# Kernel tuning notes

Hardware: AMD Instinct MI355X
Metric: run time of the kernel (lower is better)

Reference implementation:

```python
import jax, jax.numpy as jnp
import numpy as np

B = 8192
HIDDEN_DIM = 512
CODEBOOK_SIZE = 4096
ID_LENGTH = 4


def setup_inputs() -> dict:
    key = jax.random.key(0)
    kx, kc = jax.random.split(key)
    x = jax.random.normal(kx, (B, HIDDEN_DIM), dtype=jnp.float32)
    # codebooks: id_length tables of [codebook_size, hidden_dim], init ~ N(0,1) per nn.Parameter(torch.randn(...))
    codebooks = jax.random.normal(kc, (ID_LENGTH, CODEBOOK_SIZE, HIDDEN_DIM), dtype=jnp.float32)
    temperature = jnp.float32(0.05)
    return {"x": x, "temperature": temperature, "codebooks": codebooks}


def reference(x, temperature, codebooks):
    """Eval-mode forward of SemanticIDQuantizer (standard RVQ with soft/hard straight-through).
    Returns (quantized [B,D], residual_loss scalar, residuals_stack [B,L,D], codebook_usage [L,K]).
    """
    L, K, D = codebooks.shape
    temp = jnp.clip(temperature, 0.04)  # torch.clamp(temperature, min=0.04)
    residual = x
    quantized = jnp.zeros_like(x)
    residual_loss = jnp.asarray(0.0, x.dtype)
    residuals_list = []
    usage_list = []
    for i in range(L):  # small fixed layer count
        cb = codebooks[i]                                  # [K, D]
        similarity = (residual @ cb.T) / temp              # [B, K]
        hard_indices = jnp.argmax(similarity, axis=-1)     # [B]
        soft = jax.nn.softmax(similarity, axis=-1)         # [B, K]
        q_soft = soft @ cb                                 # [B, D]
        q_hard = cb[hard_indices]                          # [B, D] embedding lookup
        # straight-through: value == hard, gradient flows through soft path (and hard gather)
        q_layer = q_hard + (q_soft - jax.lax.stop_gradient(q_soft))
        residual_loss = residual_loss + jnp.mean((q_layer - residual) ** 2)
        residual = residual - q_layer
        quantized = quantized + q_layer
        residuals_list.append(residual)
        usage_list.append(jnp.zeros((K,), x.dtype).at[hard_indices].set(1.0))
    # codebook L2 regularizer: sum_i mean_k ||cb_ik||^2 * lambda / L == lambda * mean over (L,K) of ||.||^2
    codebook_reg = jnp.mean(jnp.sum(codebooks.astype(x.dtype) ** 2, axis=-1))
    residual_loss = (residual_loss + 0.01 * codebook_reg) / D
    residuals_stack = jax.lax.stop_gradient(jnp.stack(residuals_list, axis=1))  # [B, L, D]
    codebook_usage = jnp.stack(usage_list)  # [L, K]
    return quantized, residual_loss, residuals_stack, codebook_usage
```

## Files before the change

### kernel.cpp

```cpp
#include <hip/hip_runtime.h>
#include <math.h>

#define NB 8192
#define DD 512
#define KC 4096
#define NL 4

#define NTB 32
#define MARGIN_I 2048.0f
#define QS 16.0f

#define GBM 256
#define GBN 256

typedef int    i32x4 __attribute__((ext_vector_type(4)));
typedef unsigned short u16;
typedef unsigned int   u32;
typedef unsigned long long u64;

struct Top2 { float v1; int i1; float v2; int i2; };

__device__ __forceinline__ u32 umaxu(u32 a, u32 b) { return a > b ? a : b; }
__device__ __forceinline__ u32 uminu(u32 a, u32 b) { return a < b ? a : b; }

__device__ __forceinline__ u32 q8(float f) {
    int v = (int)rintf(f * QS);
    v = v < -127 ? -127 : (v > 127 ? 127 : v);
    return (u32)(v & 0xFF);
}

__global__ __launch_bounds__(256)
void k_cvt_all(const float* __restrict__ x, const float* __restrict__ cb,
               u64* __restrict__ residq, u64* __restrict__ cbq,
               double* __restrict__ cq, float* __restrict__ usage)
{
    const int bid = blockIdx.x;
    if (bid < 4096) {
        __shared__ double red[256];
        const int i = bid * 256 + threadIdx.x;
        if (bid < 64) {
            const float4 z = {0.f, 0.f, 0.f, 0.f};
            ((float4*)usage)[i] = z;
        }
        const float4 a = ((const float4*)cb)[i * 2];
        const float4 b = ((const float4*)cb)[i * 2 + 1];
        u64 p = (u64)(q8(a.x) | (q8(a.y) << 8) | (q8(a.z) << 16) | (q8(a.w) << 24))
              | ((u64)(q8(b.x) | (q8(b.y) << 8) | (q8(b.z) << 16) | (q8(b.w) << 24)) << 32);
        cbq[i] = p;
        red[threadIdx.x] = (double)a.x * a.x + (double)a.y * a.y + (double)a.z * a.z
                         + (double)a.w * a.w + (double)b.x * b.x + (double)b.y * b.y
                         + (double)b.z * b.z + (double)b.w * b.w;
        __syncthreads();
        for (int st = 128; st > 0; st >>= 1) {
            if (threadIdx.x < st) red[threadIdx.x] += red[threadIdx.x + st];
            __syncthreads();
        }
        if (threadIdx.x == 0) cq[bid] = red[0];
    } else {
        const int i = (bid - 4096) * 256 + threadIdx.x;
        const float4 a = ((const float4*)x)[i * 2];
        const float4 b = ((const float4*)x)[i * 2 + 1];
        u64 p = (u64)(q8(a.x) | (q8(a.y) << 8) | (q8(a.z) << 16) | (q8(a.w) << 24))
              | ((u64)(q8(b.x) | (q8(b.y) << 8) | (q8(b.z) << 16) | (q8(b.w) << 24)) << 32);
        residq[i] = p;
    }
}

__global__ __launch_bounds__(512, 2)
void k_simtop2(const char* __restrict__ Ri, const char* __restrict__ Ci,
               Top2* __restrict__ part )
{
    __shared__ __align__(16) char As[2][16384];
    __shared__ __align__(16) char Bs[2][16384];

    const int tid  = threadIdx.x;
    const int lane = tid & 63;
    const int w    = tid >> 6;
    const int wm   = w >> 2;
    const int wn   = w & 3;

    const int bid = blockIdx.x;
    const int xcd = bid & 7;
    const int idx = bid >> 3;
    const int row_pan  = (xcd >> 1) * 8 + (idx >> 3);
    const int col_tile = (xcd & 1) * 8 + (idx & 7);
    const int rb0 = row_pan * GBM;
    const int cb0 = col_tile * GBN;

    const int rowA = tid >> 1;
    const int h    = tid & 1;
    const int fr   = (rowA & 3) ^ ((rowA >> 2) & 3);
    const char* gAb = Ri + (size_t)(rb0 + rowA) * 512 + h * 32;
    const char* gBb = Ci + (size_t)(cb0 + rowA) * 512 + h * 32;
    const int wpos0 = rowA * 64 + (((2 * h)     ^ fr) << 4);
    const int wpos1 = rowA * 64 + (((2 * h + 1) ^ fr) << 4);

    const int la = lane & 15, ks = lane >> 4;
    const int fla = (la & 3) ^ ((la >> 2) & 3);
    const int offA = (wm * 128 + la) * 64 + ((ks ^ fla) << 4);
    const int offB = (wn * 64  + la) * 64 + ((ks ^ fla) << 4);

    i32x4 acc[8][4];
    const i32x4 zero = {0, 0, 0, 0};
#pragma unroll
    for (int m = 0; m < 8; ++m)
#pragma unroll
        for (int n = 0; n < 4; ++n) acc[m][n] = zero;

    uint4 eA0, eA1, eB0, eB1;
    uint4 oA0, oA1, oB0, oB1;

#define LOADT(rA0, rA1, rB0, rB1, T) do {                    \
        const char* _pa = gAb + (T) * 64;                    \
        rA0 = *(const uint4*)(_pa);                          \
        rA1 = *(const uint4*)(_pa + 16);                     \
        const char* _pb = gBb + (T) * 64;                    \
        rB0 = *(const uint4*)(_pb);                          \
        rB1 = *(const uint4*)(_pb + 16);                     \
    } while (0)

#define ITER(T, rA0, rA1, rB0, rB1, P) do {                               \
        *(uint4*)(&As[P][0] + wpos0) = rA0;                               \
        *(uint4*)(&As[P][0] + wpos1) = rA1;                               \
        *(uint4*)(&Bs[P][0] + wpos0) = rB0;                               \
        *(uint4*)(&Bs[P][0] + wpos1) = rB1;                               \
        if ((T) + 2 < 8) LOADT(rA0, rA1, rB0, rB1, (T) + 2);              \
        asm volatile("s_waitcnt lgkmcnt(0)" ::: "memory");                \
        __builtin_amdgcn_s_barrier();                                     \
        const char* _rA = &As[P][0];                                      \
        const char* _rB = &Bs[P][0];                                      \
        i32x4 av[8], bv[4];                                               \
        _Pragma("unroll")                                                 \
        for (int m = 0; m < 8; ++m) av[m] = *(const i32x4*)(_rA + offA + m * 1024); \
        _Pragma("unroll")                                                 \
        for (int n = 0; n < 4; ++n) bv[n] = *(const i32x4*)(_rB + offB + n * 1024); \
        _Pragma("unroll")                                                 \
        for (int m = 0; m < 8; ++m)                                       \
            _Pragma("unroll")                                             \
            for (int n = 0; n < 4; ++n)                                   \
                acc[m][n] = __builtin_amdgcn_mfma_i32_16x16x64_i8(av[m], bv[n], acc[m][n], 0, 0, 0); \
    } while (0)

    LOADT(eA0, eA1, eB0, eB1, 0);
    LOADT(oA0, oA1, oB0, oB1, 1);

#pragma unroll 1
    for (int tt = 0; tt < 8; tt += 2) {
        ITER(tt,     eA0, eA1, eB0, eB1, 0);
        ITER(tt + 1, oA0, oA1, oB0, oB1, 1);
    }
#undef ITER
#undef LOADT

    __syncthreads();
    uint2 (*mrg)[4] = (uint2 (*)[4])&As[0][0];

    const int rgrp = lane >> 4;
    const int cidx = lane & 15;
    u32 inv[4];
#pragma unroll
    for (int n = 0; n < 4; ++n)
        inv[n] = (u32)(127 - ((wn & 1) * 64 + n * 16 + cidx));

#pragma unroll
    for (int m = 0; m < 8; ++m) {
#pragma unroll
        for (int j = 0; j < 4; ++j) {
            const u32 p0 = ((((u32)acc[m][0][j]) ^ 0x80000000u) & 0xFFFFFF80u) | inv[0];
            const u32 p1 = ((((u32)acc[m][1][j]) ^ 0x80000000u) & 0xFFFFFF80u) | inv[1];
            const u32 p2 = ((((u32)acc[m][2][j]) ^ 0x80000000u) & 0xFFFFFF80u) | inv[2];
            const u32 p3 = ((((u32)acc[m][3][j]) ^ 0x80000000u) & 0xFFFFFF80u) | inv[3];
            const u32 s1 = umaxu(p0, p1), t1 = uminu(p0, p1);
            const u32 s2 = umaxu(p2, p3), t2 = uminu(p2, p3);
            u32 hi = umaxu(s1, s2);
            u32 lo = umaxu(uminu(s1, s2), umaxu(t1, t2));
#pragma unroll
            for (int off = 1; off < 16; off <<= 1) {
                const u32 oh = (u32)__shfl_xor((int)hi, off);
                const u32 ol = (u32)__shfl_xor((int)lo, off);
                const u32 nh = umaxu(hi, oh);
                lo = umaxu(uminu(hi, oh), umaxu(lo, ol));
                hi = nh;
            }
            if (cidx == 0)
                mrg[wm * 128 + m * 16 + rgrp * 4 + j][wn] = make_uint2(hi, lo);
        }
    }
    __syncthreads();
    if (tid < 256) {
#pragma unroll
        for (int tau = 0; tau < 2; ++tau) {
            const uint2 a = mrg[tid][tau * 2], b = mrg[tid][tau * 2 + 1];
            const u32 hi = umaxu(a.x, b.x);
            const u32 lo = umaxu(uminu(a.x, b.x), umaxu(a.y, b.y));
            Top2 p;
            p.v1 = (float)(int)((hi & 0xFFFFFF80u) ^ 0x80000000u);
            p.i1 = cb0 + tau * 128 + 127 - (int)(hi & 127u);
            p.v2 = (float)(int)((lo & 0xFFFFFF80u) ^ 0x80000000u);
            p.i2 = cb0 + tau * 128 + 127 - (int)(lo & 127u);
            part[(size_t)(rb0 + tid) * NTB + col_tile * 2 + tau] = p;
        }
    }
}

__global__ __launch_bounds__(256)
void k_refine(const Top2* __restrict__ part, const float* __restrict__ CB,
              const float* __restrict__ prevBase, size_t prevStride, int vecload,
              const float* __restrict__ X, float* __restrict__ out_q,
              float* __restrict__ stack, float* __restrict__ chain,
              char* __restrict__ residq, float* __restrict__ out_usage,
              float* __restrict__ pl, int layer)
{
    const int lane = threadIdx.x & 63;
    const int b    = blockIdx.x * 4 + (threadIdx.x >> 6);

    const float* pr = prevBase + (size_t)b * prevStride + lane * 8;
    float r[8];
    if (vecload) {
        const float4 a = ((const float4*)pr)[0];
        const float4 c = ((const float4*)pr)[1];
        r[0] = a.x; r[1] = a.y; r[2] = a.z; r[3] = a.w;
        r[4] = c.x; r[5] = c.y; r[6] = c.z; r[7] = c.w;
    } else {
#pragma unroll
        for (int q = 0; q < 8; ++q) r[q] = pr[q];
    }

    const uint4 pp = ((const uint4*)(part + (size_t)b * NTB))[lane >> 1];
    const float cv = (lane & 1) ? __uint_as_float(pp.z) : __uint_as_float(pp.x);
    const int   ci = (lane & 1) ? (int)pp.w : (int)pp.y;

    float mx = cv;
#pragma unroll
    for (int off = 1; off < 64; off <<= 1) mx = fmaxf(mx, __shfl_xor(mx, off));
    const float thr = mx - MARGIN_I;

    u64 mask = __ballot(cv >= thr);
    float bestV = -INFINITY;
    int   bestI = 0x7fffffff;
    while (mask) {
        const int c = __ffsll(mask) - 1;
        mask &= mask - 1;
        const int cidx = __shfl(ci, c);
        const float* cr = CB + (size_t)cidx * DD + lane * 8;
        float p = 0.f;
#pragma unroll
        for (int q = 0; q < 8; ++q) p = fmaf(r[q], cr[q], p);
#pragma unroll
        for (int off = 32; off >= 1; off >>= 1) p += __shfl_xor(p, off);
        if (p > bestV || (p == bestV && cidx < bestI)) { bestV = p; bestI = cidx; }
    }
    if (lane == 0) out_usage[layer * KC + bestI] = 1.0f;

    const float* cb = CB + (size_t)bestI * DD + lane * 8;
    float rn[8];
    float ss = 0.f;
#pragma unroll
    for (int q = 0; q < 8; ++q) { rn[q] = r[q] - cb[q]; ss = fmaf(rn[q], rn[q], ss); }

    float* sp = stack + ((size_t)b * NL + layer) * DD + lane * 8;
#pragma unroll
    for (int q = 0; q < 8; ++q) sp[q] = rn[q];

    if (chain) {
        float4 c0, c1;
        c0.x = rn[0]; c0.y = rn[1]; c0.z = rn[2]; c0.w = rn[3];
        c1.x = rn[4]; c1.y = rn[5]; c1.z = rn[6]; c1.w = rn[7];
        float4* cp = (float4*)(chain + (size_t)b * DD + lane * 8);
        cp[0] = c0; cp[1] = c1;
    }

    u64 pq = (u64)(q8(rn[0]) | (q8(rn[1]) << 8) | (q8(rn[2]) << 16) | (q8(rn[3]) << 24))
           | ((u64)(q8(rn[4]) | (q8(rn[5]) << 8) | (q8(rn[6]) << 16) | (q8(rn[7]) << 24)) << 32);
    *(u64*)(residq + (size_t)b * DD + lane * 8) = pq;

    if (layer == NL - 1) {
        const float* xr = X + (size_t)b * DD + lane * 8;
        float4 q0, q1;
        q0.x = xr[0] - rn[0]; q0.y = xr[1] - rn[1];
        q0.z = xr[2] - rn[2]; q0.w = xr[3] - rn[3];
        q1.x = xr[4] - rn[4]; q1.y = xr[5] - rn[5];
        q1.z = xr[6] - rn[6]; q1.w = xr[7] - rn[7];
        float4* qp = (float4*)(out_q + (size_t)b * DD + lane * 8);
        qp[0] = q0; qp[1] = q1;
    }

#pragma unroll
    for (int off = 32; off >= 1; off >>= 1) ss += __shfl_xor(ss, off);
    if (lane == 0) pl[(size_t)layer * NB + b] = ss;
}

__global__ __launch_bounds__(256)
void k_finalize(const float* __restrict__ pl, const double* __restrict__ cq,
                int ncq, float* __restrict__ out_loss)
{
    __shared__ double red[256];
    const int tid = threadIdx.x;
    double s = 0.0;
    for (int i = tid; i < NL * NB; i += 256) s += (double)pl[i];
    double s2 = 0.0;
    for (int i = tid; i < ncq; i += 256) s2 += cq[i];
    red[tid] = s / ((double)NB * DD) + 0.01 * (s2 / ((double)NL * KC));
    __syncthreads();
    for (int st = 128; st > 0; st >>= 1) {
        if (tid < st) red[tid] += red[tid + st];
        __syncthreads();
    }
    if (tid == 0) out_loss[0] = (float)(red[0] / (double)DD);
}

extern "C" void kernel_launch(void* const* d_in, const int* in_sizes, int n_in,
                              void* d_out, int out_size, void* d_ws, size_t ws_size,
                              hipStream_t stream)
{
    (void)in_sizes; (void)n_in; (void)out_size;
    const float* x  = (const float*)d_in[0];
    const float* cb = (const float*)d_in[2];

    float* out       = (float*)d_out;
    float* out_q     = out;
    float* out_loss  = out + (size_t)NB * DD;
    float* out_stack = out_loss + 1;
    float* out_usage = out_stack + (size_t)NB * NL * DD;

    char* ws = (char*)d_ws;
    Top2*   part   = (Top2*)ws;
    char*   residq = ws + ((size_t)4 << 20);
    char*   cbq    = ws + ((size_t)8 << 20);
    float*  pl     = (float*)(ws + ((size_t)16 << 20));
    double* cq     = (double*)(ws + ((size_t)16 << 20) + 131072 + 256);
    float*  chain  = (ws_size >= ((size_t)34 << 20))
                   ? (float*)(ws + ((size_t)17 << 20)) : nullptr;

    k_cvt_all<<<6144, 256, 0, stream>>>(x, cb, (u64*)residq, (u64*)cbq, cq, out_usage);

    for (int l = 0; l < NL; ++l) {
        const float* cbl = cb + (size_t)l * KC * DD;
        k_simtop2<<<512, 512, 0, stream>>>(residq, cbq + (size_t)l * KC * DD, part);
        const float* prevBase;
        size_t prevStride;
        int vec;
        if (l == 0)            { prevBase = x;     prevStride = DD;               vec = 1; }
        else if (chain)        { prevBase = chain; prevStride = DD;               vec = 1; }
        else                   { prevBase = out_stack + (size_t)(l - 1) * DD;
                                 prevStride = (size_t)NL * DD;                    vec = 0; }
        k_refine<<<NB / 4, 256, 0, stream>>>(part, cbl, prevBase, prevStride, vec, x,
                                             out_q, out_stack, chain, residq,
                                             out_usage, pl, l);
    }
    k_finalize<<<1, 256, 0, stream>>>(pl, cq, 4096, out_loss);
}
```

Baseline: 261.6 us.

## Restructure int8 GEMM main loop to single barrier per tile; drop chain buffer

The int8 MFMA similarity kernel's K-loop is rewritten so each tile needs one barrier instead of a store-wait-barrier sequence. Fragments are read from LDS first, then the next tile is written to the other buffer and a further global load is issued, all overlapping the MFMA block. This removes a sync stall per tile, at the cost of a deeper register-held prefetch and a hand-unrolled schedule. The top-2 merge epilogue now uses all 512 threads, one output each. The contiguous chain residual buffer is also removed, so refine reads the previous residual from the strided stack with scalar loads instead of vector loads from the chain.

```diff
diff --git a/kernel.cpp b/kernel.cpp
--- a/kernel.cpp
+++ b/kernel.cpp
@@ -119,37 +119,49 @@
         rB1 = *(const uint4*)(_pb + 16);                     \
     } while (0)
 
-#define ITER(T, rA0, rA1, rB0, rB1, P) do {                               \
-        *(uint4*)(&As[P][0] + wpos0) = rA0;                               \
-        *(uint4*)(&As[P][0] + wpos1) = rA1;                               \
-        *(uint4*)(&Bs[P][0] + wpos0) = rB0;                               \
-        *(uint4*)(&Bs[P][0] + wpos1) = rB1;                               \
-        if ((T) + 2 < 8) LOADT(rA0, rA1, rB0, rB1, (T) + 2);              \
-        asm volatile("s_waitcnt lgkmcnt(0)" ::: "memory");                \
+#define WRITET(rA0, rA1, rB0, rB1, P) do {                   \
+        *(uint4*)(&As[P][0] + wpos0) = rA0;                  \
+        *(uint4*)(&As[P][0] + wpos1) = rA1;                  \
+        *(uint4*)(&Bs[P][0] + wpos0) = rB0;                  \
+        *(uint4*)(&Bs[P][0] + wpos1) = rB1;                  \
+    } while (0)
+
+#define ITER(T, wA0, wA1, wB0, wB1, DOW, DOL) do {                        \
         __builtin_amdgcn_s_barrier();                                     \
-        const char* _rA = &As[P][0];                                      \
-        const char* _rB = &Bs[P][0];                                      \
+        __builtin_amdgcn_sched_barrier(0);                                \
+        const char* _rA = &As[(T) & 1][0];                                \
+        const char* _rB = &Bs[(T) & 1][0];                                \
         i32x4 av[8], bv[4];                                               \
         _Pragma("unroll")                                                 \
         for (int m = 0; m < 8; ++m) av[m] = *(const i32x4*)(_rA + offA + m * 1024); \
         _Pragma("unroll")                                                 \
         for (int n = 0; n < 4; ++n) bv[n] = *(const i32x4*)(_rB + offB + n * 1024); \
+        if (DOW) WRITET(wA0, wA1, wB0, wB1, ((T) + 1) & 1);               \
+        if (DOL) LOADT(wA0, wA1, wB0, wB1, (T) + 3);                      \
         _Pragma("unroll")                                                 \
         for (int m = 0; m < 8; ++m)                                       \
             _Pragma("unroll")                                             \
             for (int n = 0; n < 4; ++n)                                   \
                 acc[m][n] = __builtin_amdgcn_mfma_i32_16x16x64_i8(av[m], bv[n], acc[m][n], 0, 0, 0); \
+        asm volatile("s_waitcnt lgkmcnt(0)" ::: "memory");                \
     } while (0)
 
     LOADT(eA0, eA1, eB0, eB1, 0);
     LOADT(oA0, oA1, oB0, oB1, 1);
-
-#pragma unroll 1
-    for (int tt = 0; tt < 8; tt += 2) {
-        ITER(tt,     eA0, eA1, eB0, eB1, 0);
-        ITER(tt + 1, oA0, oA1, oB0, oB1, 1);
-    }
+    WRITET(eA0, eA1, eB0, eB1, 0);
+    LOADT(eA0, eA1, eB0, eB1, 2);
+    asm volatile("s_waitcnt lgkmcnt(0)" ::: "memory");
+
+    ITER(0, oA0, oA1, oB0, oB1, 1, 1);
+    ITER(1, eA0, eA1, eB0, eB1, 1, 1);
+    ITER(2, oA0, oA1, oB0, oB1, 1, 1);
+    ITER(3, eA0, eA1, eB0, eB1, 1, 1);
+    ITER(4, oA0, oA1, oB0, oB1, 1, 1);
+    ITER(5, eA0, eA1, eB0, eB1, 1, 0);
+    ITER(6, oA0, oA1, oB0, oB1, 1, 0);
+    ITER(7, oA0, oA1, oB0, oB1, 0, 0);
 #undef ITER
+#undef WRITET
 #undef LOADT
 
     __syncthreads();
@@ -187,44 +199,35 @@
         }
     }
     __syncthreads();
-    if (tid < 256) {
-#pragma unroll
-        for (int tau = 0; tau < 2; ++tau) {
-            const uint2 a = mrg[tid][tau * 2], b = mrg[tid][tau * 2 + 1];
-            const u32 hi = umaxu(a.x, b.x);
-            const u32 lo = umaxu(uminu(a.x, b.x), umaxu(a.y, b.y));
-            Top2 p;
-            p.v1 = (float)(int)((hi & 0xFFFFFF80u) ^ 0x80000000u);
-            p.i1 = cb0 + tau * 128 + 127 - (int)(hi & 127u);
-            p.v2 = (float)(int)((lo & 0xFFFFFF80u) ^ 0x80000000u);
-            p.i2 = cb0 + tau * 128 + 127 - (int)(lo & 127u);
-            part[(size_t)(rb0 + tid) * NTB + col_tile * 2 + tau] = p;
-        }
+    {
+        const int row = tid & 255, tau = tid >> 8;
+        const uint2 a = mrg[row][tau * 2], b = mrg[row][tau * 2 + 1];
+        const u32 hi = umaxu(a.x, b.x);
+        const u32 lo = umaxu(uminu(a.x, b.x), umaxu(a.y, b.y));
+        Top2 p;
+        p.v1 = (float)(int)((hi & 0xFFFFFF80u) ^ 0x80000000u);
+        p.i1 = cb0 + tau * 128 + 127 - (int)(hi & 127u);
+        p.v2 = (float)(int)((lo & 0xFFFFFF80u) ^ 0x80000000u);
+        p.i2 = cb0 + tau * 128 + 127 - (int)(lo & 127u);
+        part[(size_t)(rb0 + row) * NTB + col_tile * 2 + tau] = p;
     }
 }
 
 __global__ __launch_bounds__(256)
 void k_refine(const Top2* __restrict__ part, const float* __restrict__ CB,
-              const float* __restrict__ prevBase, size_t prevStride, int vecload,
+              const float* __restrict__ prevBase, size_t prevStride,
               const float* __restrict__ X, float* __restrict__ out_q,
-              float* __restrict__ stack, float* __restrict__ chain,
-              char* __restrict__ residq, float* __restrict__ out_usage,
-              float* __restrict__ pl, int layer)
+              float* __restrict__ stack, char* __restrict__ residq,
+              float* __restrict__ out_usage, float* __restrict__ pl,
+              int layer)
 {
     const int lane = threadIdx.x & 63;
     const int b    = blockIdx.x * 4 + (threadIdx.x >> 6);
 
     const float* pr = prevBase + (size_t)b * prevStride + lane * 8;
     float r[8];
-    if (vecload) {
-        const float4 a = ((const float4*)pr)[0];
-        const float4 c = ((const float4*)pr)[1];
-        r[0] = a.x; r[1] = a.y; r[2] = a.z; r[3] = a.w;
-        r[4] = c.x; r[5] = c.y; r[6] = c.z; r[7] = c.w;
-    } else {
-#pragma unroll
-        for (int q = 0; q < 8; ++q) r[q] = pr[q];
-    }
+#pragma unroll
+    for (int q = 0; q < 8; ++q) r[q] = pr[q];
 
     const uint4 pp = ((const uint4*)(part + (size_t)b * NTB))[lane >> 1];
     const float cv = (lane & 1) ? __uint_as_float(pp.z) : __uint_as_float(pp.x);
@@ -261,14 +264,6 @@
     float* sp = stack + ((size_t)b * NL + layer) * DD + lane * 8;
 #pragma unroll
     for (int q = 0; q < 8; ++q) sp[q] = rn[q];
-
-    if (chain) {
-        float4 c0, c1;
-        c0.x = rn[0]; c0.y = rn[1]; c0.z = rn[2]; c0.w = rn[3];
-        c1.x = rn[4]; c1.y = rn[5]; c1.z = rn[6]; c1.w = rn[7];
-        float4* cp = (float4*)(chain + (size_t)b * DD + lane * 8);
-        cp[0] = c0; cp[1] = c1;
-    }
 
     u64 pq = (u64)(q8(rn[0]) | (q8(rn[1]) << 8) | (q8(rn[2]) << 16) | (q8(rn[3]) << 24))
            | ((u64)(q8(rn[4]) | (q8(rn[5]) << 8) | (q8(rn[6]) << 16) | (q8(rn[7]) << 24)) << 32);
@@ -313,7 +308,7 @@
                               void* d_out, int out_size, void* d_ws, size_t ws_size,
                               hipStream_t stream)
 {
-    (void)in_sizes; (void)n_in; (void)out_size;
+    (void)in_sizes; (void)n_in; (void)out_size; (void)ws_size;
     const float* x  = (const float*)d_in[0];
     const float* cb = (const float*)d_in[2];
 
@@ -329,24 +324,16 @@
     char*   cbq    = ws + ((size_t)8 << 20);
     float*  pl     = (float*)(ws + ((size_t)16 << 20));
     double* cq     = (double*)(ws + ((size_t)16 << 20) + 131072 + 256);
-    float*  chain  = (ws_size >= ((size_t)34 << 20))
-                   ? (float*)(ws + ((size_t)17 << 20)) : nullptr;
 
     k_cvt_all<<<6144, 256, 0, stream>>>(x, cb, (u64*)residq, (u64*)cbq, cq, out_usage);
 
     for (int l = 0; l < NL; ++l) {
         const float* cbl = cb + (size_t)l * KC * DD;
         k_simtop2<<<512, 512, 0, stream>>>(residq, cbq + (size_t)l * KC * DD, part);
-        const float* prevBase;
-        size_t prevStride;
-        int vec;
-        if (l == 0)            { prevBase = x;     prevStride = DD;               vec = 1; }
-        else if (chain)        { prevBase = chain; prevStride = DD;               vec = 1; }
-        else                   { prevBase = out_stack + (size_t)(l - 1) * DD;
-                                 prevStride = (size_t)NL * DD;                    vec = 0; }
-        k_refine<<<NB / 4, 256, 0, stream>>>(part, cbl, prevBase, prevStride, vec, x,
-                                             out_q, out_stack, chain, residq,
-                                             out_usage, pl, l);
+        const float* prevBase = (l == 0) ? x : (out_stack + (size_t)(l - 1) * DD);
+        const size_t prevStride = (l == 0) ? (size_t)DD : (size_t)NL * DD;
+        k_refine<<<NB / 4, 256, 0, stream>>>(part, cbl, prevBase, prevStride, x, out_q,
+                                             out_stack, residq, out_usage, pl, l);
     }
     k_finalize<<<1, 256, 0, stream>>>(pl, cq, 4096, out_loss);
 }
```

Measured after the change: 253.9 us. 1.03x faster.
